# Kernel optimization log

Measured on AMD Instinct MI355X. Metric: run time of the kernel, lower is better.

Reference implementation:

```python
import jax, jax.numpy as jnp
import numpy as np

B, T, DM = 1, 8192, 1024
DS, DC, EXP = 16, 4, 2
DI = DM * EXP  # 2048


def setup_inputs() -> dict:
    key = jax.random.key(0)
    ks = jax.random.split(key, 6)
    sc = lambda k, shape, s: jax.random.normal(k, shape, jnp.float32) * s
    return {
        "x": jax.random.normal(ks[0], (B, T, DM), jnp.float32),
        "W_in": sc(ks[1], (DM, 2 * DI), 0.02),        # stored [in, out]
        "conv_w": sc(ks[2], (DI, 1, DC), 0.2),        # depthwise conv weight (OIH)
        "conv_b": jnp.zeros((DI,), jnp.float32),
        "W_x": sc(ks[3], (DI, 2 * DS + 1), 0.02),     # stored [in, out]
        "A_log": jnp.log(jnp.arange(1, DS + 1, dtype=jnp.float32)),
        "D": jnp.ones((DI,), jnp.float32),
        "W_out": sc(ks[4], (DI, DM), 0.02),           # stored [in, out]
    }


def reference(x, W_in, conv_w, conv_b, W_x, A_log, D, W_out):
    Bq, Tq, _ = x.shape
    # input projection and gate split
    xz = x @ W_in                              # [B,T,2*DI]
    xc, z = jnp.split(xz, 2, axis=-1)          # each [B,T,DI]
    # causal depthwise conv1d (pad left DC-1 == torch pad both + truncate [:T])
    xcT = jnp.transpose(xc, (0, 2, 1))         # [B,DI,T]
    conv = jax.lax.conv_general_dilated(
        xcT, conv_w, window_strides=(1,), padding=[(DC - 1, 0)],
        feature_group_count=DI)
    conv = conv + conv_b[None, :, None]
    xs = jax.nn.silu(jnp.transpose(conv, (0, 2, 1)))   # [B,T,DI]
    # selective SSM parameters (single shared delta per timestep)
    x_dbl = xs @ W_x                           # [B,T,2N+1]
    delta = jax.nn.softplus(x_dbl[..., :1])    # [B,T,1]
    Bp = x_dbl[..., 1:1 + DS]                  # [B,T,N]
    Cp = x_dbl[..., 1 + DS:]                   # [B,T,N]
    A = -jnp.exp(A_log)                        # [N]
    A_bar = jnp.exp(delta * A)                 # [B,T,N]
    B_bar = delta * Bp                         # [B,T,N]

    def step(h, inp):
        a_t, b_t, x_t, c_t = inp               # [B,N],[B,N],[B,DI],[B,N]
        h = a_t[:, None, :] * h + b_t[:, None, :] * x_t[:, :, None]  # [B,DI,N]
        y_t = jnp.einsum('bdn,bn->bd', h, c_t)
        return h, y_t

    h0 = jnp.zeros((Bq, DI, DS), xs.dtype)
    seq = (jnp.swapaxes(A_bar, 0, 1), jnp.swapaxes(B_bar, 0, 1),
           jnp.swapaxes(xs, 0, 1), jnp.swapaxes(Cp, 0, 1))
    _, ys = jax.lax.scan(step, h0, seq)        # ys: [T,B,DI]
    y = jnp.swapaxes(ys, 0, 1) + D * xs        # [B,T,DI]
    y = y * jax.nn.silu(z)
    return y @ W_out                           # [B,T,DM]
```

## Files before the change

### kernel.cpp

```cpp
#include <hip/hip_runtime.h>
#include <hip/hip_bf16.h>

#define T_SEQ 8192
#define DMODEL 1024
#define DINNER 2048
#define NSTATE 16
#define NCH 128
#define CL 64

typedef __attribute__((ext_vector_type(8))) short bf16x8;
typedef __attribute__((ext_vector_type(4))) float f32x4;

__device__ __forceinline__ float bf2f(ushort u) {
  union { unsigned u; float f; } c; c.u = ((unsigned)u) << 16; return c.f;
}
__device__ __forceinline__ ushort f2bf(float f) {
  union { float f; unsigned u; } c; c.f = f;
  unsigned r = c.u + 0x7FFFu + ((c.u >> 16) & 1u);
  return (ushort)(r >> 16);
}

#define GLD16(dst, src) __builtin_amdgcn_global_load_lds( \
    (const __attribute__((address_space(1))) void*)(src), \
    (__attribute__((address_space(3))) void*)(dst), 16, 0, 0)

template<int N> __device__ __forceinline__ void waitcnt_vm() {
  asm volatile("s_waitcnt vmcnt(%0)" :: "i"(N) : "memory");
}

__global__ __launch_bounds__(256) void cast_bf16(const float* __restrict__ in,
                                                 ushort* __restrict__ out, int n4) {
  int i = blockIdx.x * 256 + threadIdx.x;
  if (i < n4) {
    float4 v = ((const float4*)in)[i];
    ushort4 o;
    o.x = f2bf(v.x); o.y = f2bf(v.y); o.z = f2bf(v.z); o.w = f2bf(v.w);
    ((ushort4*)out)[i] = o;
  }
}

__global__ __launch_bounds__(256) void transpose_bf16(const float* __restrict__ in,
                                                      ushort* __restrict__ out, int R, int C) {
  __shared__ float tile[32][33];
  int bx = blockIdx.x * 32;
  int by = blockIdx.y * 32;
  int x = threadIdx.x, y = threadIdx.y;
#pragma unroll
  for (int j = 0; j < 32; j += 8)
    tile[y + j][x] = in[(size_t)(by + y + j) * C + bx + x];
  __syncthreads();
#pragma unroll
  for (int j = 0; j < 32; j += 8)
    out[(size_t)(bx + y + j) * R + by + x] = f2bf(tile[x][y + j]);
}

__global__ __launch_bounds__(256) void wx_transpose_pad(const float* __restrict__ Wx,
                                                        ushort* __restrict__ wxT) {
  int idx = blockIdx.x * 256 + threadIdx.x;
  int j = idx >> 11;
  int k = idx & 2047;
  wxT[idx] = (j < 33) ? f2bf(Wx[k * 33 + j]) : (ushort)0;
}

template<int BF16OUT, int MW, int NW, int MR, int NR>
__global__ __launch_bounds__(512, 2)
void gemm_pipe(const ushort* __restrict__ A, const ushort* __restrict__ B,
               void* __restrict__ Cout, int N, int K, int nbn) {
  constexpr int BM = MW * MR * 16;
  constexpr int BN = NW * NR * 16;
  constexpr int RA = BM / 128;
  constexpr int RB = BN / 128;
  constexpr int L  = RA + RB;
  extern __shared__ __align__(16) char smem[];
  char* const sB = smem + 4 * BM * 64;

  const int tid = threadIdx.x, lane = tid & 63, wid = tid >> 6;
  const int wm = wid / NW, wn = wid % NW;

  const int nwg = gridDim.x;
  const int q = nwg >> 3, r = nwg & 7;
  const int xcd = blockIdx.x & 7, bidx = blockIdx.x >> 3;
  const int wg = (xcd < r ? xcd * (q + 1) : r * (q + 1) + (xcd - r) * q) + bidx;
  const int mbase = (wg / nbn) * BM;
  const int nbase = (wg % nbn) * BN;
  const int NT = K >> 5;

  const int srow = tid >> 2;
  const int scol = ((tid & 3) ^ (srow & 3)) << 3;
  const ushort* pa[RA];
  const ushort* pb[RB];
#pragma unroll
  for (int j = 0; j < RA; ++j) pa[j] = A + (size_t)(mbase + j * 128 + srow) * K + scol;
#pragma unroll
  for (int j = 0; j < RB; ++j) pb[j] = B + (size_t)(nbase + j * 128 + srow) * K + scol;

  auto stageA = [&](int tt) {
    char* d = smem + (tt & 3) * (BM * 64) + wid * 1024;
#pragma unroll
    for (int j = 0; j < RA; ++j) GLD16(d + j * 8192, pa[j] + tt * 32);
  };
  auto stageB = [&](int tt) {
    char* d = sB + (tt & 3) * (BN * 64) + wid * 1024;
#pragma unroll
    for (int j = 0; j < RB; ++j) GLD16(d + j * 8192, pb[j] + tt * 32);
  };

  const int frow = lane & 15;
  const int gsw = (((lane >> 4) ^ (frow & 3)) << 4);
  const int aoff0 = (wm * MR * 16 + frow) * 64 + gsw;
  const int boff0 = (wn * NR * 16 + frow) * 64 + gsw;

  f32x4 acc[MR][NR];
#pragma unroll
  for (int m = 0; m < MR; ++m)
#pragma unroll
    for (int n = 0; n < NR; ++n) acc[m][n] = (f32x4){0.f, 0.f, 0.f, 0.f};

#pragma unroll
  for (int tt = 0; tt < 3; ++tt) if (tt < NT) { stageA(tt); stageB(tt); }
  waitcnt_vm<2 * L>();
  __builtin_amdgcn_s_barrier();

  for (int t = 0; t < NT; ++t) {
    const char* bufA = smem + (t & 3) * (BM * 64);
    const char* bufB = sB + (t & 3) * (BN * 64);
    bf16x8 af[MR], bfr[NR];
#pragma unroll
    for (int m = 0; m < MR; ++m) af[m] = *(const bf16x8*)(bufA + aoff0 + m * 1024);
#pragma unroll
    for (int n = 0; n < NR; ++n) bfr[n] = *(const bf16x8*)(bufB + boff0 + n * 1024);
    if (t + 3 < NT) stageA(t + 3);
    __builtin_amdgcn_s_barrier();
    asm volatile("s_waitcnt lgkmcnt(0)" ::: "memory");
    __builtin_amdgcn_s_setprio(1);
#pragma unroll
    for (int m = 0; m < MR / 2; ++m)
#pragma unroll
      for (int n = 0; n < NR; ++n)
        acc[m][n] = __builtin_amdgcn_mfma_f32_16x16x32_bf16(af[m], bfr[n], acc[m][n], 0, 0, 0);
    __builtin_amdgcn_s_setprio(0);
    __builtin_amdgcn_s_barrier();
    if (t + 3 < NT) stageB(t + 3);
    __builtin_amdgcn_s_setprio(1);
#pragma unroll
    for (int m = MR / 2; m < MR; ++m)
#pragma unroll
      for (int n = 0; n < NR; ++n)
        acc[m][n] = __builtin_amdgcn_mfma_f32_16x16x32_bf16(af[m], bfr[n], acc[m][n], 0, 0, 0);
    __builtin_amdgcn_s_setprio(0);
    if (t + 4 <= NT)      waitcnt_vm<2 * L>();
    else if (t + 3 <= NT) waitcnt_vm<L>();
    else if (t + 2 <= NT) waitcnt_vm<0>();
    __builtin_amdgcn_s_barrier();
  }

  const int crow0 = mbase + wm * MR * 16 + (lane >> 4) * 4;
  const int ccol0 = nbase + wn * NR * 16 + (lane & 15);
#pragma unroll
  for (int m = 0; m < MR; ++m)
#pragma unroll
    for (int n = 0; n < NR; ++n)
#pragma unroll
      for (int j = 0; j < 4; ++j) {
        int rr = crow0 + m * 16 + j;
        int cc = ccol0 + n * 16;
        float v = acc[m][n][j];
        if (BF16OUT) ((ushort*)Cout)[(size_t)rr * N + cc] = f2bf(v);
        else         ((float*) Cout)[(size_t)rr * N + cc] = v;
      }
}

__global__ __launch_bounds__(256) void gemm_thin(const ushort* __restrict__ A,
                                                 const ushort* __restrict__ Bw,
                                                 float* __restrict__ part) {
  __shared__ __align__(16) ushort sA[128 * 64];
  __shared__ __align__(16) ushort sB[48 * 64];
  const int tid = threadIdx.x, lane = tid & 63, wid = tid >> 6;
  const int mbase = blockIdx.x * 128;
  const int kbase = blockIdx.y * 512;
  const int frow = lane & 15, fke = (lane >> 4) * 8;

  f32x4 acc[2][3];
#pragma unroll
  for (int m = 0; m < 2; ++m)
#pragma unroll
    for (int n = 0; n < 3; ++n) acc[m][n] = (f32x4){0.f, 0.f, 0.f, 0.f};

  for (int k0 = 0; k0 < 512; k0 += 64) {
#pragma unroll
    for (int j = 0; j < 4; ++j) {
      int o = tid * 16 + j * 4096;
      int row = o >> 7, ke = ((o >> 4) & 7) * 8;
      GLD16((char*)sA + wid * 1024 + j * 4096,
            A + (size_t)(mbase + row) * DINNER + kbase + k0 + ke);
    }
    for (int i = tid; i < 384; i += 256) {
      int brow = i >> 3, kc = (i & 7) * 8;
      *(bf16x8*)&sB[brow * 64 + kc] = *(const bf16x8*)(Bw + (size_t)brow * DINNER + kbase + k0 + kc);
    }
    __syncthreads();
    bf16x8 af[2][2], bf_[3][2];
#pragma unroll
    for (int m = 0; m < 2; ++m)
#pragma unroll
      for (int ks = 0; ks < 2; ++ks)
        af[m][ks] = *(const bf16x8*)&sA[(wid * 32 + m * 16 + frow) * 64 + ks * 32 + fke];
#pragma unroll
    for (int n = 0; n < 3; ++n)
#pragma unroll
      for (int ks = 0; ks < 2; ++ks)
        bf_[n][ks] = *(const bf16x8*)&sB[(n * 16 + frow) * 64 + ks * 32 + fke];
#pragma unroll
    for (int m = 0; m < 2; ++m)
#pragma unroll
      for (int n = 0; n < 3; ++n)
#pragma unroll
        for (int ks = 0; ks < 2; ++ks)
          acc[m][n] = __builtin_amdgcn_mfma_f32_16x16x32_bf16(af[m][ks], bf_[n][ks], acc[m][n], 0, 0, 0);
    __syncthreads();
  }
  float* po = part + (size_t)blockIdx.y * (T_SEQ * 48);
#pragma unroll
  for (int m = 0; m < 2; ++m)
#pragma unroll
    for (int n = 0; n < 3; ++n)
#pragma unroll
      for (int j = 0; j < 4; ++j) {
        int rr = mbase + wid * 32 + m * 16 + (lane >> 4) * 4 + j;
        int cc = n * 16 + (lane & 15);
        po[(size_t)rr * 48 + cc] = acc[m][n][j];
      }
}

__global__ __launch_bounds__(256) void reduce4(const float* __restrict__ part,
                                               float* __restrict__ xdbl) {
  int i = blockIdx.x * 256 + threadIdx.x;
  const float4* p = (const float4*)part;
  float4 a = p[i], b = p[i + 98304], c = p[i + 2 * 98304], d = p[i + 3 * 98304];
  ((float4*)xdbl)[i] = make_float4(a.x + b.x + c.x + d.x, a.y + b.y + c.y + d.y,
                                   a.z + b.z + c.z + d.z, a.w + b.w + c.w + d.w);
}

__global__ __launch_bounds__(256) void conv_silu(const ushort* __restrict__ xz,
                                                 const float* __restrict__ cw,
                                                 const float* __restrict__ cb,
                                                 ushort* __restrict__ xs) {
  int idx = blockIdx.x * 256 + threadIdx.x;
  int t = idx >> 11, d = idx & 2047;
  float4 w = *(const float4*)(cw + d * 4);
  float a = cb[d];
  const float wk[4] = {w.x, w.y, w.z, w.w};
#pragma unroll
  for (int k = 0; k < 4; ++k) {
    int tt = t - 3 + k;
    if (tt >= 0) a += bf2f(xz[(size_t)tt * 4096 + d]) * wk[k];
  }
  float s = a / (1.f + expf(-a));
  xs[idx] = f2bf(s);
}

__global__ __launch_bounds__(256) void precompute_k(const float* __restrict__ xdbl,
                                                    const float* __restrict__ A_log,
                                                    float* __restrict__ abar,
                                                    float* __restrict__ bbar,
                                                    float* __restrict__ cc,
                                                    float* __restrict__ dlt) {
  int t = blockIdx.x * 256 + threadIdx.x;
  if (t >= T_SEQ) return;
  const float* r = xdbl + (size_t)t * 48;
  float v = r[0];
  float delta = (v > 20.f) ? v : log1pf(expf(v));
  dlt[t] = delta;
#pragma unroll
  for (int n = 0; n < NSTATE; ++n) {
    float A = -expf(A_log[n]);
    abar[t * 16 + n] = expf(delta * A);
    bbar[t * 16 + n] = delta * r[1 + n];
    cc[t * 16 + n]   = r[17 + n];
  }
}

__global__ __launch_bounds__(256) void chunkprod_k(const float* __restrict__ dlt,
                                                   const float* __restrict__ A_log,
                                                   float* __restrict__ P) {
  int idx = blockIdx.x * 256 + threadIdx.x;
  if (idx >= NCH * NSTATE) return;
  int c = idx >> 4, n = idx & 15;
  float s = 0.f;
  for (int i = 0; i < CL; ++i) s += dlt[c * CL + i];
  P[idx] = expf(-expf(A_log[n]) * s);
}

__global__ __launch_bounds__(256) void scan1(const ushort* __restrict__ xs,
                                             const float* __restrict__ abar,
                                             const float* __restrict__ bbar,
                                             float* __restrict__ hend) {
  int c = blockIdx.x;
  int d = blockIdx.y * 256 + threadIdx.x;
  __shared__ float s_ab[CL * 16], s_bb[CL * 16];
  for (int e = threadIdx.x; e < CL * 16; e += 256) {
    s_ab[e] = abar[(size_t)c * CL * 16 + e];
    s_bb[e] = bbar[(size_t)c * CL * 16 + e];
  }
  __syncthreads();
  float h[16];
#pragma unroll
  for (int n = 0; n < 16; ++n) h[n] = 0.f;
  int tbase = c * CL;
  for (int i = 0; i < CL; ++i) {
    float x = bf2f(xs[(size_t)(tbase + i) * DINNER + d]);
#pragma unroll
    for (int n = 0; n < 16; ++n) h[n] = s_ab[i * 16 + n] * h[n] + s_bb[i * 16 + n] * x;
  }
  float* o = hend + ((size_t)c * DINNER + d) * 16;
#pragma unroll
  for (int qq = 0; qq < 4; ++qq)
    ((float4*)o)[qq] = make_float4(h[4 * qq], h[4 * qq + 1], h[4 * qq + 2], h[4 * qq + 3]);
}

__global__ __launch_bounds__(256) void scan2(const float* __restrict__ hend,
                                             const float* __restrict__ P,
                                             float* __restrict__ hin) {
  int idx = blockIdx.x * 256 + threadIdx.x;
  int n = idx & 15;
  float h = 0.f;
  for (int c = 0; c < NCH; ++c) {
    hin[(size_t)c * (DINNER * 16) + idx] = h;
    h = P[c * 16 + n] * h + hend[(size_t)c * (DINNER * 16) + idx];
  }
}

__global__ __launch_bounds__(256) void scan3(const ushort* __restrict__ xs,
                                             const ushort* __restrict__ xz,
                                             const float* __restrict__ abar,
                                             const float* __restrict__ bbar,
                                             const float* __restrict__ cc,
                                             const float* __restrict__ hin,
                                             const float* __restrict__ Dv,
                                             ushort* __restrict__ y) {
  int c = blockIdx.x;
  int d = blockIdx.y * 256 + threadIdx.x;
  __shared__ float s_ab[CL * 16], s_bb[CL * 16], s_cc[CL * 16];
  for (int e = threadIdx.x; e < CL * 16; e += 256) {
    s_ab[e] = abar[(size_t)c * CL * 16 + e];
    s_bb[e] = bbar[(size_t)c * CL * 16 + e];
    s_cc[e] = cc[(size_t)c * CL * 16 + e];
  }
  __syncthreads();
  float h[16];
  const float* hi = hin + ((size_t)c * DINNER + d) * 16;
#pragma unroll
  for (int qq = 0; qq < 4; ++qq) {
    float4 v = ((const float4*)hi)[qq];
    h[4 * qq] = v.x; h[4 * qq + 1] = v.y; h[4 * qq + 2] = v.z; h[4 * qq + 3] = v.w;
  }
  float Dd = Dv[d];
  int tbase = c * CL;
  for (int i = 0; i < CL; ++i) {
    size_t t = tbase + i;
    float x = bf2f(xs[t * DINNER + d]);
    float ys = 0.f;
#pragma unroll
    for (int n = 0; n < 16; ++n) {
      h[n] = s_ab[i * 16 + n] * h[n] + s_bb[i * 16 + n] * x;
      ys += s_cc[i * 16 + n] * h[n];
    }
    float z = bf2f(xz[t * 4096 + 2048 + d]);
    float yv = (ys + Dd * x) * (z / (1.f + expf(-z)));
    y[t * DINNER + d] = f2bf(yv);
  }
}

extern "C" void kernel_launch(void* const* d_in, const int* in_sizes, int n_in,
                              void* d_out, int out_size, void* d_ws, size_t ws_size,
                              hipStream_t stream) {
  const float* x      = (const float*)d_in[0];
  const float* W_in   = (const float*)d_in[1];
  const float* conv_w = (const float*)d_in[2];
  const float* conv_b = (const float*)d_in[3];
  const float* W_x    = (const float*)d_in[4];
  const float* A_log  = (const float*)d_in[5];
  const float* Dv     = (const float*)d_in[6];
  const float* W_out  = (const float*)d_in[7];
  float* out = (float*)d_out;

  char* w = (char*)d_ws;
  auto alloc = [&](size_t bytes) { char* p = w; w += (bytes + 255) & ~(size_t)255; return p; };

  ushort* xbf   = (ushort*)alloc((size_t)T_SEQ * DMODEL * 2);
  ushort* winT  = (ushort*)alloc((size_t)4096 * 1024 * 2);
  ushort* woutT = (ushort*)alloc((size_t)1024 * 2048 * 2);
  ushort* wxT   = (ushort*)alloc((size_t)48 * 2048 * 2);
  ushort* xz    = (ushort*)alloc((size_t)T_SEQ * 4096 * 2);
  ushort* xs    = (ushort*)alloc((size_t)T_SEQ * DINNER * 2);
  float*  xdbl  = (float*) alloc((size_t)T_SEQ * 48 * 4);
  float*  parts = (float*) alloc((size_t)4 * T_SEQ * 48 * 4);
  float*  abar  = (float*) alloc((size_t)T_SEQ * 16 * 4);
  float*  bbar  = (float*) alloc((size_t)T_SEQ * 16 * 4);
  float*  ccb   = (float*) alloc((size_t)T_SEQ * 16 * 4);
  float*  dlt   = (float*) alloc((size_t)T_SEQ * 4);
  float*  P     = (float*) alloc((size_t)NCH * 16 * 4);
  float*  hend  = (float*) alloc((size_t)NCH * DINNER * 16 * 4);
  float*  hin   = (float*) alloc((size_t)NCH * DINNER * 16 * 4);
  ushort* ybf   = (ushort*)alloc((size_t)T_SEQ * DINNER * 2);

  auto kg1 = gemm_pipe<1, 2, 4, 8, 4>;
  auto kg3 = gemm_pipe<0, 4, 2, 4, 4>;
  hipFuncSetAttribute(reinterpret_cast<const void*>(kg1),
                      hipFuncAttributeMaxDynamicSharedMemorySize, 131072);
  hipFuncSetAttribute(reinterpret_cast<const void*>(kg3),
                      hipFuncAttributeMaxDynamicSharedMemorySize, 98304);

  cast_bf16<<<(T_SEQ * DMODEL / 4 + 255) / 256, 256, 0, stream>>>(x, xbf, T_SEQ * DMODEL / 4);
  transpose_bf16<<<dim3(4096 / 32, 1024 / 32), dim3(32, 8), 0, stream>>>(W_in, winT, 1024, 4096);
  transpose_bf16<<<dim3(1024 / 32, 2048 / 32), dim3(32, 8), 0, stream>>>(W_out, woutT, 2048, 1024);
  wx_transpose_pad<<<(48 * 2048) / 256, 256, 0, stream>>>(W_x, wxT);

  kg1<<<dim3((T_SEQ / 256) * (4096 / 256)), 512, 131072, stream>>>(xbf, winT, xz, 4096, 1024, 4096 / 256);

  conv_silu<<<(T_SEQ * DINNER) / 256, 256, 0, stream>>>(xz, conv_w, conv_b, xs);

  gemm_thin<<<dim3(T_SEQ / 128, 4), 256, 0, stream>>>(xs, wxT, parts);
  reduce4<<<(T_SEQ * 48 / 4) / 256, 256, 0, stream>>>(parts, xdbl);

  precompute_k<<<T_SEQ / 256, 256, 0, stream>>>(xdbl, A_log, abar, bbar, ccb, dlt);
  chunkprod_k<<<(NCH * 16 + 255) / 256, 256, 0, stream>>>(dlt, A_log, P);

  scan1<<<dim3(NCH, DINNER / 256), 256, 0, stream>>>(xs, abar, bbar, hend);
  scan2<<<(DINNER * 16) / 256, 256, 0, stream>>>(hend, P, hin);
  scan3<<<dim3(NCH, DINNER / 256), 256, 0, stream>>>(xs, xz, abar, bbar, ccb, hin, Dv, ybf);

  kg3<<<dim3((T_SEQ / 256) * (1024 / 128)), 512, 98304, stream>>>(ybf, woutT, out, 1024, 2048, 1024 / 128);
}
```

Baseline: 310.4 us.

## Rework bf16 GEMM into 256x128 tiles with BK=64, 3-stage buffering and quadrant-phased MFMA

The templated GEMM becomes a fixed 256x128 tile kernel with a K step of 64, a triple-buffered LDS ring, 128-byte XOR swizzling, and four compute phases per iteration that interleave LDS fragment loads and async global-to-LDS prefetch with MFMA groups. The aim is to overlap memory traffic with tensor-core work and use fewer barriers per unit of K for both the input and output projections. The input projection now writes xc and z into separate contiguous buffers, so conv_silu and scan3 read with a 2048 stride. In exchange, LDS use grows to 144KB, which may limit occupancy, and the first GEMM's tile shape changes from 256x256.

```diff
diff --git a/kernel.cpp b/kernel.cpp
--- a/kernel.cpp
+++ b/kernel.cpp
@@ -27,6 +27,8 @@
 template<int N> __device__ __forceinline__ void waitcnt_vm() {
   asm volatile("s_waitcnt vmcnt(%0)" :: "i"(N) : "memory");
 }
+#define LGKM0() do { asm volatile("s_waitcnt lgkmcnt(0)" ::: "memory"); \
+                     __builtin_amdgcn_sched_barrier(0); } while (0)
 
 __global__ __launch_bounds__(256) void cast_bf16(const float* __restrict__ in,
                                                  ushort* __restrict__ out, int n4) {
@@ -62,112 +64,164 @@
   wxT[idx] = (j < 33) ? f2bf(Wx[k * 33 + j]) : (ushort)0;
 }
 
-template<int BF16OUT, int MW, int NW, int MR, int NR>
+template<int OUTMODE>
 __global__ __launch_bounds__(512, 2)
 void gemm_pipe(const ushort* __restrict__ A, const ushort* __restrict__ B,
-               void* __restrict__ Cout, int N, int K, int nbn) {
-  constexpr int BM = MW * MR * 16;
-  constexpr int BN = NW * NR * 16;
-  constexpr int RA = BM / 128;
-  constexpr int RB = BN / 128;
-  constexpr int L  = RA + RB;
+               void* __restrict__ out0, void* __restrict__ out1,
+               int N, int K, int nbn) {
   extern __shared__ __align__(16) char smem[];
-  char* const sB = smem + 4 * BM * 64;
+  char* const smemB = smem + 98304;
 
   const int tid = threadIdx.x, lane = tid & 63, wid = tid >> 6;
-  const int wm = wid / NW, wn = wid % NW;
+  const int wm = wid >> 1, wn = wid & 1;
 
   const int nwg = gridDim.x;
   const int q = nwg >> 3, r = nwg & 7;
   const int xcd = blockIdx.x & 7, bidx = blockIdx.x >> 3;
   const int wg = (xcd < r ? xcd * (q + 1) : r * (q + 1) + (xcd - r) * q) + bidx;
-  const int mbase = (wg / nbn) * BM;
-  const int nbase = (wg % nbn) * BN;
-  const int NT = K >> 5;
-
-  const int srow = tid >> 2;
-  const int scol = ((tid & 3) ^ (srow & 3)) << 3;
-  const ushort* pa[RA];
-  const ushort* pb[RB];
-#pragma unroll
-  for (int j = 0; j < RA; ++j) pa[j] = A + (size_t)(mbase + j * 128 + srow) * K + scol;
-#pragma unroll
-  for (int j = 0; j < RB; ++j) pb[j] = B + (size_t)(nbase + j * 128 + srow) * K + scol;
-
-  auto stageA = [&](int tt) {
-    char* d = smem + (tt & 3) * (BM * 64) + wid * 1024;
-#pragma unroll
-    for (int j = 0; j < RA; ++j) GLD16(d + j * 8192, pa[j] + tt * 32);
-  };
-  auto stageB = [&](int tt) {
-    char* d = sB + (tt & 3) * (BN * 64) + wid * 1024;
-#pragma unroll
-    for (int j = 0; j < RB; ++j) GLD16(d + j * 8192, pb[j] + tt * 32);
-  };
-
-  const int frow = lane & 15;
-  const int gsw = (((lane >> 4) ^ (frow & 3)) << 4);
-  const int aoff0 = (wm * MR * 16 + frow) * 64 + gsw;
-  const int boff0 = (wn * NR * 16 + frow) * 64 + gsw;
-
-  f32x4 acc[MR][NR];
-#pragma unroll
-  for (int m = 0; m < MR; ++m)
-#pragma unroll
-    for (int n = 0; n < NR; ++n) acc[m][n] = (f32x4){0.f, 0.f, 0.f, 0.f};
-
-#pragma unroll
-  for (int tt = 0; tt < 3; ++tt) if (tt < NT) { stageA(tt); stageB(tt); }
-  waitcnt_vm<2 * L>();
+  const int mbase = (wg / nbn) * 256;
+  const int nbase = (wg % nbn) * 128;
+  const int NT = K >> 6;
+
+  const int srow = tid >> 3;
+  const int scb = ((tid & 7) << 4) ^ ((srow & 7) << 4);
+  const ushort* pa[4];
+  const ushort* pb[2];
+#pragma unroll
+  for (int j = 0; j < 4; ++j) pa[j] = A + (size_t)(mbase + j * 64 + srow) * K + (scb >> 1);
+#pragma unroll
+  for (int j = 0; j < 2; ++j) pb[j] = B + (size_t)(nbase + j * 64 + srow) * K + (scb >> 1);
+
+#define STA(buf, j, tt) GLD16(smem  + (buf) * 32768 + (j) * 8192 + wid * 1024, pa[j] + (size_t)(tt) * 64)
+#define STB(buf, j, tt) GLD16(smemB + (buf) * 16384 + (j) * 8192 + wid * 1024, pb[j] + (size_t)(tt) * 64)
+
+  const int frow = lane & 15, hh = lane >> 4;
+  const int cbk0 = (hh << 4) ^ ((frow & 7) << 4);
+  const int cbk1 = (64 + (hh << 4)) ^ ((frow & 7) << 4);
+  const int arow0 = (wm * 64 + frow) * 128;
+  const int brow0 = (wn * 64 + frow) * 128;
+
+  f32x4 acc[4][4];
+#pragma unroll
+  for (int m = 0; m < 4; ++m)
+#pragma unroll
+    for (int n = 0; n < 4; ++n) acc[m][n] = (f32x4){0.f, 0.f, 0.f, 0.f};
+
+#pragma unroll
+  for (int tt = 0; tt < 2; ++tt) {
+    STA(tt, 0, tt); STA(tt, 1, tt); STA(tt, 2, tt); STA(tt, 3, tt);
+    STB(tt, 0, tt); STB(tt, 1, tt);
+  }
+  waitcnt_vm<6>();
   __builtin_amdgcn_s_barrier();
 
+  int cur = 0;
   for (int t = 0; t < NT; ++t) {
-    const char* bufA = smem + (t & 3) * (BM * 64);
-    const char* bufB = sB + (t & 3) * (BN * 64);
-    bf16x8 af[MR], bfr[NR];
-#pragma unroll
-    for (int m = 0; m < MR; ++m) af[m] = *(const bf16x8*)(bufA + aoff0 + m * 1024);
-#pragma unroll
-    for (int n = 0; n < NR; ++n) bfr[n] = *(const bf16x8*)(bufB + boff0 + n * 1024);
-    if (t + 3 < NT) stageA(t + 3);
-    __builtin_amdgcn_s_barrier();
-    asm volatile("s_waitcnt lgkmcnt(0)" ::: "memory");
+    const char* bA = smem + cur * 32768;
+    const char* bB = smemB + cur * 16384;
+    const int nxt = cur + 2 - ((cur >= 1) ? 3 : 0);
+    const bool pf = (t + 2 < NT);
+    bf16x8 alo[2][2], ahi[2][2], blo[2][2], bhi[2][2];
+
+#pragma unroll
+    for (int m = 0; m < 2; ++m) {
+      alo[m][0] = *(const bf16x8*)(bA + arow0 + m * 2048 + cbk0);
+      alo[m][1] = *(const bf16x8*)(bA + arow0 + m * 2048 + cbk1);
+    }
+#pragma unroll
+    for (int n = 0; n < 2; ++n) {
+      blo[n][0] = *(const bf16x8*)(bB + brow0 + n * 2048 + cbk0);
+      blo[n][1] = *(const bf16x8*)(bB + brow0 + n * 2048 + cbk1);
+    }
+    if (pf) { STA(nxt, 0, t + 2); STA(nxt, 1, t + 2); }
+    __builtin_amdgcn_s_barrier();
+    LGKM0();
     __builtin_amdgcn_s_setprio(1);
 #pragma unroll
-    for (int m = 0; m < MR / 2; ++m)
-#pragma unroll
-      for (int n = 0; n < NR; ++n)
-        acc[m][n] = __builtin_amdgcn_mfma_f32_16x16x32_bf16(af[m], bfr[n], acc[m][n], 0, 0, 0);
+    for (int m = 0; m < 2; ++m)
+#pragma unroll
+      for (int n = 0; n < 2; ++n)
+#pragma unroll
+        for (int kk = 0; kk < 2; ++kk)
+          acc[m][n] = __builtin_amdgcn_mfma_f32_16x16x32_bf16(alo[m][kk], blo[n][kk], acc[m][n], 0, 0, 0);
     __builtin_amdgcn_s_setprio(0);
     __builtin_amdgcn_s_barrier();
-    if (t + 3 < NT) stageB(t + 3);
+
+#pragma unroll
+    for (int m = 0; m < 2; ++m) {
+      ahi[m][0] = *(const bf16x8*)(bA + arow0 + (2 + m) * 2048 + cbk0);
+      ahi[m][1] = *(const bf16x8*)(bA + arow0 + (2 + m) * 2048 + cbk1);
+    }
+    if (pf) { STA(nxt, 2, t + 2); STA(nxt, 3, t + 2); }
+    __builtin_amdgcn_s_barrier();
+    LGKM0();
     __builtin_amdgcn_s_setprio(1);
 #pragma unroll
-    for (int m = MR / 2; m < MR; ++m)
-#pragma unroll
-      for (int n = 0; n < NR; ++n)
-        acc[m][n] = __builtin_amdgcn_mfma_f32_16x16x32_bf16(af[m], bfr[n], acc[m][n], 0, 0, 0);
+    for (int m = 0; m < 2; ++m)
+#pragma unroll
+      for (int n = 0; n < 2; ++n)
+#pragma unroll
+        for (int kk = 0; kk < 2; ++kk)
+          acc[2 + m][n] = __builtin_amdgcn_mfma_f32_16x16x32_bf16(ahi[m][kk], blo[n][kk], acc[2 + m][n], 0, 0, 0);
     __builtin_amdgcn_s_setprio(0);
-    if (t + 4 <= NT)      waitcnt_vm<2 * L>();
-    else if (t + 3 <= NT) waitcnt_vm<L>();
-    else if (t + 2 <= NT) waitcnt_vm<0>();
-    __builtin_amdgcn_s_barrier();
-  }
-
-  const int crow0 = mbase + wm * MR * 16 + (lane >> 4) * 4;
-  const int ccol0 = nbase + wn * NR * 16 + (lane & 15);
-#pragma unroll
-  for (int m = 0; m < MR; ++m)
-#pragma unroll
-    for (int n = 0; n < NR; ++n)
+    __builtin_amdgcn_s_barrier();
+
+#pragma unroll
+    for (int n = 0; n < 2; ++n) {
+      bhi[n][0] = *(const bf16x8*)(bB + brow0 + (2 + n) * 2048 + cbk0);
+      bhi[n][1] = *(const bf16x8*)(bB + brow0 + (2 + n) * 2048 + cbk1);
+    }
+    if (pf) STB(nxt, 0, t + 2);
+    __builtin_amdgcn_s_barrier();
+    LGKM0();
+    __builtin_amdgcn_s_setprio(1);
+#pragma unroll
+    for (int m = 0; m < 2; ++m)
+#pragma unroll
+      for (int n = 0; n < 2; ++n)
+#pragma unroll
+        for (int kk = 0; kk < 2; ++kk)
+          acc[2 + m][2 + n] = __builtin_amdgcn_mfma_f32_16x16x32_bf16(ahi[m][kk], bhi[n][kk], acc[2 + m][2 + n], 0, 0, 0);
+    __builtin_amdgcn_s_setprio(0);
+    __builtin_amdgcn_s_barrier();
+
+    if (pf) STB(nxt, 1, t + 2);
+    __builtin_amdgcn_s_setprio(1);
+#pragma unroll
+    for (int m = 0; m < 2; ++m)
+#pragma unroll
+      for (int n = 0; n < 2; ++n)
+#pragma unroll
+        for (int kk = 0; kk < 2; ++kk)
+          acc[m][2 + n] = __builtin_amdgcn_mfma_f32_16x16x32_bf16(alo[m][kk], bhi[n][kk], acc[m][2 + n], 0, 0, 0);
+    __builtin_amdgcn_s_setprio(0);
+    if (pf) waitcnt_vm<6>(); else waitcnt_vm<0>();
+    __builtin_amdgcn_s_barrier();
+
+    cur = cur + 1 - ((cur == 2) ? 3 : 0);
+  }
+
+  const int crow0 = mbase + wm * 64 + (lane >> 4) * 4;
+  const int ccol0 = nbase + wn * 64 + (lane & 15);
+#pragma unroll
+  for (int m = 0; m < 4; ++m)
+#pragma unroll
+    for (int n = 0; n < 4; ++n)
 #pragma unroll
       for (int j = 0; j < 4; ++j) {
         int rr = crow0 + m * 16 + j;
         int cc = ccol0 + n * 16;
         float v = acc[m][n][j];
-        if (BF16OUT) ((ushort*)Cout)[(size_t)rr * N + cc] = f2bf(v);
-        else         ((float*) Cout)[(size_t)rr * N + cc] = v;
+        if (OUTMODE == 0) {
+          ((float*)out0)[(size_t)rr * N + cc] = v;
+        } else {
+          ushort* dst = (cc < 2048) ? (ushort*)out0 : (ushort*)out1;
+          int c2 = cc & 2047;
+          dst[(size_t)rr * 2048 + c2] = f2bf(v);
+        }
       }
+#undef STA
+#undef STB
 }
 
 __global__ __launch_bounds__(256) void gemm_thin(const ushort* __restrict__ A,
@@ -241,7 +295,7 @@
                                    a.z + b.z + c.z + d.z, a.w + b.w + c.w + d.w);
 }
 
-__global__ __launch_bounds__(256) void conv_silu(const ushort* __restrict__ xz,
+__global__ __launch_bounds__(256) void conv_silu(const ushort* __restrict__ xc,
                                                  const float* __restrict__ cw,
                                                  const float* __restrict__ cb,
                                                  ushort* __restrict__ xs) {
@@ -253,7 +307,7 @@
 #pragma unroll
   for (int k = 0; k < 4; ++k) {
     int tt = t - 3 + k;
-    if (tt >= 0) a += bf2f(xz[(size_t)tt * 4096 + d]) * wk[k];
+    if (tt >= 0) a += bf2f(xc[(size_t)tt * 2048 + d]) * wk[k];
   }
   float s = a / (1.f + expf(-a));
   xs[idx] = f2bf(s);
@@ -331,7 +385,7 @@
 }
 
 __global__ __launch_bounds__(256) void scan3(const ushort* __restrict__ xs,
-                                             const ushort* __restrict__ xz,
+                                             const ushort* __restrict__ zb,
                                              const float* __restrict__ abar,
                                              const float* __restrict__ bbar,
                                              const float* __restrict__ cc,
@@ -365,7 +419,7 @@
       h[n] = s_ab[i * 16 + n] * h[n] + s_bb[i * 16 + n] * x;
       ys += s_cc[i * 16 + n] * h[n];
     }
-    float z = bf2f(xz[t * 4096 + 2048 + d]);
+    float z = bf2f(zb[t * 2048 + d]);
     float yv = (ys + Dd * x) * (z / (1.f + expf(-z)));
     y[t * DINNER + d] = f2bf(yv);
   }
@@ -391,7 +445,8 @@
   ushort* winT  = (ushort*)alloc((size_t)4096 * 1024 * 2);
   ushort* woutT = (ushort*)alloc((size_t)1024 * 2048 * 2);
   ushort* wxT   = (ushort*)alloc((size_t)48 * 2048 * 2);
-  ushort* xz    = (ushort*)alloc((size_t)T_SEQ * 4096 * 2);
+  ushort* xc    = (ushort*)alloc((size_t)T_SEQ * DINNER * 2);
+  ushort* zb    = (ushort*)alloc((size_t)T_SEQ * DINNER * 2);
   ushort* xs    = (ushort*)alloc((size_t)T_SEQ * DINNER * 2);
   float*  xdbl  = (float*) alloc((size_t)T_SEQ * 48 * 4);
   float*  parts = (float*) alloc((size_t)4 * T_SEQ * 48 * 4);
@@ -404,21 +459,21 @@
   float*  hin   = (float*) alloc((size_t)NCH * DINNER * 16 * 4);
   ushort* ybf   = (ushort*)alloc((size_t)T_SEQ * DINNER * 2);
 
-  auto kg1 = gemm_pipe<1, 2, 4, 8, 4>;
-  auto kg3 = gemm_pipe<0, 4, 2, 4, 4>;
+  auto kg1 = gemm_pipe<1>;
+  auto kg3 = gemm_pipe<0>;
   hipFuncSetAttribute(reinterpret_cast<const void*>(kg1),
-                      hipFuncAttributeMaxDynamicSharedMemorySize, 131072);
+                      hipFuncAttributeMaxDynamicSharedMemorySize, 147456);
   hipFuncSetAttribute(reinterpret_cast<const void*>(kg3),
-                      hipFuncAttributeMaxDynamicSharedMemorySize, 98304);
+                      hipFuncAttributeMaxDynamicSharedMemorySize, 147456);
 
   cast_bf16<<<(T_SEQ * DMODEL / 4 + 255) / 256, 256, 0, stream>>>(x, xbf, T_SEQ * DMODEL / 4);
   transpose_bf16<<<dim3(4096 / 32, 1024 / 32), dim3(32, 8), 0, stream>>>(W_in, winT, 1024, 4096);
   transpose_bf16<<<dim3(1024 / 32, 2048 / 32), dim3(32, 8), 0, stream>>>(W_out, woutT, 2048, 1024);
   wx_transpose_pad<<<(48 * 2048) / 256, 256, 0, stream>>>(W_x, wxT);
 
-  kg1<<<dim3((T_SEQ / 256) * (4096 / 256)), 512, 131072, stream>>>(xbf, winT, xz, 4096, 1024, 4096 / 256);
-
-  conv_silu<<<(T_SEQ * DINNER) / 256, 256, 0, stream>>>(xz, conv_w, conv_b, xs);
+  kg1<<<dim3((T_SEQ / 256) * (4096 / 128)), 512, 147456, stream>>>(xbf, winT, xc, zb, 4096, 1024, 4096 / 128);
+
+  conv_silu<<<(T_SEQ * DINNER) / 256, 256, 0, stream>>>(xc, conv_w, conv_b, xs);
 
   gemm_thin<<<dim3(T_SEQ / 128, 4), 256, 0, stream>>>(xs, wxT, parts);
   reduce4<<<(T_SEQ * 48 / 4) / 256, 256, 0, stream>>>(parts, xdbl);
@@ -428,7 +483,7 @@
 
   scan1<<<dim3(NCH, DINNER / 256), 256, 0, stream>>>(xs, abar, bbar, hend);
   scan2<<<(DINNER * 16) / 256, 256, 0, stream>>>(hend, P, hin);
-  scan3<<<dim3(NCH, DINNER / 256), 256, 0, stream>>>(xs, xz, abar, bbar, ccb, hin, Dv, ybf);
-
-  kg3<<<dim3((T_SEQ / 256) * (1024 / 128)), 512, 98304, stream>>>(ybf, woutT, out, 1024, 2048, 1024 / 128);
-}
+  scan3<<<dim3(NCH, DINNER / 256), 256, 0, stream>>>(xs, zb, abar, bbar, ccb, hin, Dv, ybf);
+
+  kg3<<<dim3((T_SEQ / 256) * (1024 / 128)), 512, 147456, stream>>>(ybf, woutT, out, nullptr, 1024, 2048, 1024 / 128);
+}
```

After: 316.8 us. +2.1%, slower.
